# Kernel tuning notes

Measured on AMD Instinct MI355X. Metric: run time of the kernel, lower is better.

Reference implementation:

```python
import jax, jax.numpy as jnp
import numpy as np

B, H, Q, D = 8, 32, 1, 128
MAX_SEQ = 4096


def setup_inputs() -> dict:
    key = jax.random.key(0)
    k1, k2, k3, k4, k5 = jax.random.split(key, 5)
    return {
        "query": jax.random.normal(k1, (B, H, Q, D), dtype=jnp.float32),
        "key": jax.random.normal(k2, (B, H, Q, D), dtype=jnp.float32),
        "value": jax.random.normal(k3, (B, H, Q, D), dtype=jnp.float32),
        "cache_k": jax.random.normal(k4, (B, H, MAX_SEQ, D), dtype=jnp.float32),
        "cache_v": jax.random.normal(k5, (B, H, MAX_SEQ, D), dtype=jnp.float32),
        "cache_pos": MAX_SEQ - 1,  # decode step: cache nearly full
    }


def reference(query, key, value, cache_k, cache_v, cache_pos):
    # cache_pos is a static Python int (decode-step position, > 0).
    new_seq_len = key.shape[2]
    end_pos = cache_pos + new_seq_len
    # Slice-write new K/V into the cache (the torch module's in-place write).
    cache_k = cache_k.at[:, :, cache_pos:end_pos, :].set(key)
    cache_v = cache_v.at[:, :, cache_pos:end_pos, :].set(value)
    # Contiguous view of the valid prefix (the torch .contiguous() copy).
    full_k = cache_k[:, :, :end_pos, :]  # [B, H, end_pos, D]
    full_v = cache_v[:, :, :end_pos, :]
    # Decode path: SDPA with no mask, not causal.
    scale = 1.0 / jnp.sqrt(jnp.asarray(query.shape[-1], query.dtype))
    scores = jnp.einsum("bhqd,bhkd->bhqk", query, full_k) * scale
    attn = jax.nn.softmax(scores, axis=-1)
    out = jnp.einsum("bhqk,bhkd->bhqd", attn, full_v)
    return out
```

## Files before the change

### kernel.cpp

```cpp
#include <hip/hip_runtime.h>
#include <math.h>


#define BH_     256
#define D_      128
#define MAXS_   4096
#define NSPLIT_ 8
#define CHUNK_  (MAXS_ / NSPLIT_)
#define NWAVES_ 4
#define KPW_    (CHUNK_ / NWAVES_)
#define NPART_  (NWAVES_ * 2)
#define PSTRIDE_ (D_ + 2)

typedef float f4n __attribute__((ext_vector_type(4)));

static __device__ __forceinline__ f4n ntld4(const float* p) {
    return __builtin_nontemporal_load((const f4n*)p);
}

__global__ __launch_bounds__(256) void attn_partial_kernel(
    const float* __restrict__ q,
    const float* __restrict__ ck,
    const float* __restrict__ cv,
    const int*   __restrict__ cpos_p,
    float*       __restrict__ part)
{
    const int bh    = blockIdx.x;
    const int split = blockIdx.y;
    const int wave  = threadIdx.x >> 6;
    const int lane  = threadIdx.x & 63;
    const int half  = lane >> 5;
    const int li    = lane & 31;

    const int cpos = cpos_p[0];

    const float scale = 0.08838834764831845f;

    f4n qv = *(const f4n*)(q + (size_t)bh * D_ + li * 4);
    qv *= scale;

    const int base  = split * CHUNK_ + wave * KPW_;
    int limit = cpos - base;
    limit = limit < 0 ? 0 : (limit > KPW_ ? KPW_ : limit);

    float m = -INFINITY;
    float l = 0.0f;
    f4n   o = {0.0f, 0.0f, 0.0f, 0.0f};

    const float* __restrict__ kbase = ck + (size_t)bh * MAXS_ * D_;
    const float* __restrict__ vbase = cv + (size_t)bh * MAXS_ * D_;

#define UPDATE(KV, VV)                                                   \
    do {                                                                 \
        float dp = (KV).x * qv.x + (KV).y * qv.y                         \
                 + (KV).z * qv.z + (KV).w * qv.w;                        \
        dp += __shfl_xor(dp, 16);                                        \
        dp += __shfl_xor(dp, 8);                                         \
        dp += __shfl_xor(dp, 4);                                         \
        dp += __shfl_xor(dp, 2);                                         \
        dp += __shfl_xor(dp, 1);                                         \
        const float mn   = fmaxf(m, dp);                                 \
        const float corr = __expf(m - mn);                               \
        const float p    = __expf(dp - mn);                              \
        l   = l   * corr + p;                                            \
        o.x = o.x * corr + p * (VV).x;                                   \
        o.y = o.y * corr + p * (VV).y;                                   \
        o.z = o.z * corr + p * (VV).z;                                   \
        o.w = o.w * corr + p * (VV).w;                                   \
        m = mn;                                                          \
    } while (0)

    if (limit == KPW_) {
        const float* kp = kbase + (size_t)base * D_ + lane * 4;
        const float* vp = vbase + (size_t)base * D_ + lane * 4;
        f4n ka = ntld4(kp),        va = ntld4(vp);
        f4n kb = ntld4(kp + 256),  vb = ntld4(vp + 256);
        kp += 512; vp += 512;
        for (int i = 0; i < 31; ++i) {
            const f4n kc = ntld4(kp),       vc = ntld4(vp);
            const f4n kd = ntld4(kp + 256), vd = ntld4(vp + 256);
            kp += 512; vp += 512;
            UPDATE(ka, va);
            UPDATE(kb, vb);
            ka = kc; va = vc; kb = kd; vb = vd;
        }
        UPDATE(ka, va);
        UPDATE(kb, vb);
    } else {
        const int npairs = limit >> 1;
        for (int i = 0; i < npairs; ++i) {
            const int s0 = base + i * 2;
            const f4n kv = ntld4(kbase + (size_t)s0 * D_ + lane * 4);
            const f4n vv = ntld4(vbase + (size_t)s0 * D_ + lane * 4);
            UPDATE(kv, vv);
        }
        if ((limit & 1) && half == 0) {
            const int s = base + limit - 1;
            const f4n kv = ntld4(kbase + (size_t)s * D_ + li * 4);
            const f4n vv = ntld4(vbase + (size_t)s * D_ + li * 4);
            UPDATE(kv, vv);
        }
    }
#undef UPDATE

    __shared__ float s_o[NPART_][D_];
    __shared__ float s_m[NPART_];
    __shared__ float s_l[NPART_];
    const int pi = wave * 2 + half;
    *(f4n*)&s_o[pi][li * 4] = o;
    if (li == 0) { s_m[pi] = m; s_l[pi] = l; }
    __syncthreads();

    if (wave == 0) {
        float M = -INFINITY;
        #pragma unroll
        for (int p = 0; p < NPART_; ++p) M = fmaxf(M, s_m[p]);

        float* pp = part + ((size_t)bh * NSPLIT_ + split) * PSTRIDE_;
        const int d0 = lane * 2;
        if (M == -INFINITY) {
            pp[d0]     = 0.0f;
            pp[d0 + 1] = 0.0f;
            if (lane == 0) { pp[D_] = -INFINITY; pp[D_ + 1] = 0.0f; }
        } else {
            float L = 0.0f, a0 = 0.0f, a1 = 0.0f;
            #pragma unroll
            for (int p = 0; p < NPART_; ++p) {
                const float mp = s_m[p];
                const float w  = (mp == -INFINITY) ? 0.0f : __expf(mp - M);
                L  += w * s_l[p];
                a0 += w * s_o[p][d0];
                a1 += w * s_o[p][d0 + 1];
            }
            pp[d0]     = a0;
            pp[d0 + 1] = a1;
            if (lane == 0) { pp[D_] = M; pp[D_ + 1] = L; }
        }
    }
}

__global__ __launch_bounds__(64) void attn_combine_kernel(
    const float* __restrict__ q,
    const float* __restrict__ knew,
    const float* __restrict__ vnew,
    const float* __restrict__ part,
    float*       __restrict__ out)
{
    const int bh   = blockIdx.x;
    const int lane = threadIdx.x;
    const float scale = 0.08838834764831845f;

    const float2 qv = *(const float2*)(q    + (size_t)bh * D_ + lane * 2);
    const float2 kn = *(const float2*)(knew + (size_t)bh * D_ + lane * 2);
    float dp = qv.x * kn.x + qv.y * kn.y;
    #pragma unroll
    for (int off = 32; off > 0; off >>= 1) dp += __shfl_xor(dp, off);
    const float sc = dp * scale;

    const float* pb = part + (size_t)bh * NSPLIT_ * PSTRIDE_;

    float M = sc;
    #pragma unroll
    for (int p = 0; p < NSPLIT_; ++p) M = fmaxf(M, pb[p * PSTRIDE_ + D_]);

    const int d0 = lane * 2;
    const float2 vn = *(const float2*)(vnew + (size_t)bh * D_ + d0);
    const float wn = __expf(sc - M);
    float L  = wn;
    float a0 = wn * vn.x;
    float a1 = wn * vn.y;
    #pragma unroll
    for (int p = 0; p < NSPLIT_; ++p) {
        const float mp = pb[p * PSTRIDE_ + D_];
        const float w  = (mp == -INFINITY) ? 0.0f : __expf(mp - M);
        L  += w * pb[p * PSTRIDE_ + D_ + 1];
        a0 += w * pb[p * PSTRIDE_ + d0];
        a1 += w * pb[p * PSTRIDE_ + d0 + 1];
    }
    out[(size_t)bh * D_ + d0]     = a0 / L;
    out[(size_t)bh * D_ + d0 + 1] = a1 / L;
}

extern "C" void kernel_launch(void* const* d_in, const int* in_sizes, int n_in,
                              void* d_out, int out_size, void* d_ws, size_t ws_size,
                              hipStream_t stream) {
    const float* q    = (const float*)d_in[0];
    const float* knew = (const float*)d_in[1];
    const float* vnew = (const float*)d_in[2];
    const float* ck   = (const float*)d_in[3];
    const float* cv   = (const float*)d_in[4];
    const int*   cpos = (const int*)d_in[5];
    float* out  = (float*)d_out;
    float* part = (float*)d_ws;

    dim3 grid1(BH_, NSPLIT_);
    attn_partial_kernel<<<grid1, 256, 0, stream>>>(q, ck, cv, cpos, part);
    attn_combine_kernel<<<BH_, 64, 0, stream>>>(q, knew, vnew, part, out);
}
```

Measured before the change: 180.5 us.

## Fuse split-K partial and combine kernels into one 1024-thread block per head

```diff
diff --git a/kernel.cpp b/kernel.cpp
--- a/kernel.cpp
+++ b/kernel.cpp
@@ -2,15 +2,12 @@
 #include <math.h>
 
 
-#define BH_     256
-#define D_      128
-#define MAXS_   4096
-#define NSPLIT_ 8
-#define CHUNK_  (MAXS_ / NSPLIT_)
-#define NWAVES_ 4
-#define KPW_    (CHUNK_ / NWAVES_)
-#define NPART_  (NWAVES_ * 2)
-#define PSTRIDE_ (D_ + 2)
+#define BH_   256
+#define D_    128
+#define MAXS_ 4096
+#define NW_   16
+#define KPW_  (MAXS_ / NW_)
+#define NPART_ (NW_ * 2)
 
 typedef float f4n __attribute__((ext_vector_type(4)));
 
@@ -18,19 +15,20 @@
     return __builtin_nontemporal_load((const f4n*)p);
 }
 
-__global__ __launch_bounds__(256) void attn_partial_kernel(
+__global__ __launch_bounds__(1024) void attn_fused_kernel(
     const float* __restrict__ q,
+    const float* __restrict__ knew,
+    const float* __restrict__ vnew,
     const float* __restrict__ ck,
     const float* __restrict__ cv,
     const int*   __restrict__ cpos_p,
-    float*       __restrict__ part)
+    float*       __restrict__ out)
 {
-    const int bh    = blockIdx.x;
-    const int split = blockIdx.y;
-    const int wave  = threadIdx.x >> 6;
-    const int lane  = threadIdx.x & 63;
-    const int half  = lane >> 5;
-    const int li    = lane & 31;
+    const int bh   = blockIdx.x;
+    const int wave = threadIdx.x >> 6;
+    const int lane = threadIdx.x & 63;
+    const int half = lane >> 5;
+    const int li   = lane & 31;
 
     const int cpos = cpos_p[0];
 
@@ -39,7 +37,7 @@
     f4n qv = *(const f4n*)(q + (size_t)bh * D_ + li * 4);
     qv *= scale;
 
-    const int base  = split * CHUNK_ + wave * KPW_;
+    const int base  = wave * KPW_;
     int limit = cpos - base;
     limit = limit < 0 ? 0 : (limit > KPW_ ? KPW_ : limit);
 
@@ -76,7 +74,7 @@
         f4n ka = ntld4(kp),        va = ntld4(vp);
         f4n kb = ntld4(kp + 256),  vb = ntld4(vp + 256);
         kp += 512; vp += 512;
-        for (int i = 0; i < 31; ++i) {
+        for (int i = 0; i < (KPW_ / 4) - 1; ++i) {
             const f4n kc = ntld4(kp),       vc = ntld4(vp);
             const f4n kd = ntld4(kp + 256), vd = ntld4(vp + 256);
             kp += 512; vp += 512;
@@ -112,73 +110,33 @@
     __syncthreads();
 
     if (wave == 0) {
-        float M = -INFINITY;
+        const float2 q2 = *(const float2*)(q    + (size_t)bh * D_ + lane * 2);
+        const float2 k2 = *(const float2*)(knew + (size_t)bh * D_ + lane * 2);
+        float dp = q2.x * k2.x + q2.y * k2.y;
+        #pragma unroll
+        for (int off = 32; off > 0; off >>= 1) dp += __shfl_xor(dp, off);
+        const float sc = dp * scale;
+
+        float M = sc;
         #pragma unroll
         for (int p = 0; p < NPART_; ++p) M = fmaxf(M, s_m[p]);
 
-        float* pp = part + ((size_t)bh * NSPLIT_ + split) * PSTRIDE_;
         const int d0 = lane * 2;
-        if (M == -INFINITY) {
-            pp[d0]     = 0.0f;
-            pp[d0 + 1] = 0.0f;
-            if (lane == 0) { pp[D_] = -INFINITY; pp[D_ + 1] = 0.0f; }
-        } else {
-            float L = 0.0f, a0 = 0.0f, a1 = 0.0f;
-            #pragma unroll
-            for (int p = 0; p < NPART_; ++p) {
-                const float mp = s_m[p];
-                const float w  = (mp == -INFINITY) ? 0.0f : __expf(mp - M);
-                L  += w * s_l[p];
-                a0 += w * s_o[p][d0];
-                a1 += w * s_o[p][d0 + 1];
-            }
-            pp[d0]     = a0;
-            pp[d0 + 1] = a1;
-            if (lane == 0) { pp[D_] = M; pp[D_ + 1] = L; }
+        const float2 vn = *(const float2*)(vnew + (size_t)bh * D_ + d0);
+        const float wn = __expf(sc - M);
+        float L  = wn;
+        float a0 = wn * vn.x;
+        float a1 = wn * vn.y;
+        #pragma unroll
+        for (int p = 0; p < NPART_; ++p) {
+            const float w = __expf(s_m[p] - M);
+            L  += w * s_l[p];
+            a0 += w * s_o[p][d0];
+            a1 += w * s_o[p][d0 + 1];
         }
+        out[(size_t)bh * D_ + d0]     = a0 / L;
+        out[(size_t)bh * D_ + d0 + 1] = a1 / L;
     }
-}
-
-__global__ __launch_bounds__(64) void attn_combine_kernel(
-    const float* __restrict__ q,
-    const float* __restrict__ knew,
-    const float* __restrict__ vnew,
-    const float* __restrict__ part,
-    float*       __restrict__ out)
-{
-    const int bh   = blockIdx.x;
-    const int lane = threadIdx.x;
-    const float scale = 0.08838834764831845f;
-
-    const float2 qv = *(const float2*)(q    + (size_t)bh * D_ + lane * 2);
-    const float2 kn = *(const float2*)(knew + (size_t)bh * D_ + lane * 2);
-    float dp = qv.x * kn.x + qv.y * kn.y;
-    #pragma unroll
-    for (int off = 32; off > 0; off >>= 1) dp += __shfl_xor(dp, off);
-    const float sc = dp * scale;
-
-    const float* pb = part + (size_t)bh * NSPLIT_ * PSTRIDE_;
-
-    float M = sc;
-    #pragma unroll
-    for (int p = 0; p < NSPLIT_; ++p) M = fmaxf(M, pb[p * PSTRIDE_ + D_]);
-
-    const int d0 = lane * 2;
-    const float2 vn = *(const float2*)(vnew + (size_t)bh * D_ + d0);
-    const float wn = __expf(sc - M);
-    float L  = wn;
-    float a0 = wn * vn.x;
-    float a1 = wn * vn.y;
-    #pragma unroll
-    for (int p = 0; p < NSPLIT_; ++p) {
-        const float mp = pb[p * PSTRIDE_ + D_];
-        const float w  = (mp == -INFINITY) ? 0.0f : __expf(mp - M);
-        L  += w * pb[p * PSTRIDE_ + D_ + 1];
-        a0 += w * pb[p * PSTRIDE_ + d0];
-        a1 += w * pb[p * PSTRIDE_ + d0 + 1];
-    }
-    out[(size_t)bh * D_ + d0]     = a0 / L;
-    out[(size_t)bh * D_ + d0 + 1] = a1 / L;
 }
 
 extern "C" void kernel_launch(void* const* d_in, const int* in_sizes, int n_in,
@@ -190,10 +148,7 @@
     const float* ck   = (const float*)d_in[3];
     const float* cv   = (const float*)d_in[4];
     const int*   cpos = (const int*)d_in[5];
-    float* out  = (float*)d_out;
-    float* part = (float*)d_ws;
+    float* out = (float*)d_out;
 
-    dim3 grid1(BH_, NSPLIT_);
-    attn_partial_kernel<<<grid1, 256, 0, stream>>>(q, ck, cv, cpos, part);
-    attn_combine_kernel<<<BH_, 64, 0, stream>>>(q, knew, vnew, part, out);
+    attn_fused_kernel<<<BH_, NW_ * 64, 0, stream>>>(q, knew, vnew, ck, cv, cpos, out);
 }
```

Result: slower. 197.5 us (+9.4%).

## Fuse combine into partial kernel via last-block atomic counter

Applied to the files above, without the earlier changes.

```diff
diff --git a/kernel.cpp b/kernel.cpp
--- a/kernel.cpp
+++ b/kernel.cpp
@@ -11,6 +11,7 @@
 #define KPW_    (CHUNK_ / NWAVES_)
 #define NPART_  (NWAVES_ * 2)
 #define PSTRIDE_ (D_ + 2)
+#define PART_BYTES_ ((size_t)BH_ * NSPLIT_ * PSTRIDE_ * 4)
 
 typedef float f4n __attribute__((ext_vector_type(4)));
 
@@ -18,12 +19,16 @@
     return __builtin_nontemporal_load((const f4n*)p);
 }
 
-__global__ __launch_bounds__(256) void attn_partial_kernel(
+__global__ __launch_bounds__(256, 8) void attn_partial_fused_kernel(
     const float* __restrict__ q,
+    const float* __restrict__ knew,
+    const float* __restrict__ vnew,
     const float* __restrict__ ck,
     const float* __restrict__ cv,
     const int*   __restrict__ cpos_p,
-    float*       __restrict__ part)
+    float*       __restrict__ part,
+    unsigned int* __restrict__ ctr,
+    float*       __restrict__ out)
 {
     const int bh    = blockIdx.x;
     const int split = blockIdx.y;
@@ -76,7 +81,7 @@
         f4n ka = ntld4(kp),        va = ntld4(vp);
         f4n kb = ntld4(kp + 256),  vb = ntld4(vp + 256);
         kp += 512; vp += 512;
-        for (int i = 0; i < 31; ++i) {
+        for (int i = 0; i < (KPW_ / 4) - 1; ++i) {
             const f4n kc = ntld4(kp),       vc = ntld4(vp);
             const f4n kd = ntld4(kp + 256), vd = ntld4(vp + 256);
             kp += 512; vp += 512;
@@ -111,7 +116,9 @@
     if (li == 0) { s_m[pi] = m; s_l[pi] = l; }
     __syncthreads();
 
-    if (wave == 0) {
+    if (wave != 0) return;
+
+    {
         float M = -INFINITY;
         #pragma unroll
         for (int p = 0; p < NPART_; ++p) M = fmaxf(M, s_m[p]);
@@ -137,22 +144,18 @@
             if (lane == 0) { pp[D_] = M; pp[D_ + 1] = L; }
         }
     }
-}
-
-__global__ __launch_bounds__(64) void attn_combine_kernel(
-    const float* __restrict__ q,
-    const float* __restrict__ knew,
-    const float* __restrict__ vnew,
-    const float* __restrict__ part,
-    float*       __restrict__ out)
-{
-    const int bh   = blockIdx.x;
-    const int lane = threadIdx.x;
-    const float scale = 0.08838834764831845f;
-
-    const float2 qv = *(const float2*)(q    + (size_t)bh * D_ + lane * 2);
+
+    __threadfence();
+    int old = 0;
+    if (lane == 0) old = (int)atomicAdd(&ctr[bh], 1u);
+    old = __shfl(old, 0);
+    if (old != NSPLIT_ - 1) return;
+
+    __threadfence();
+
+    const float2 q2 = *(const float2*)(q    + (size_t)bh * D_ + lane * 2);
     const float2 kn = *(const float2*)(knew + (size_t)bh * D_ + lane * 2);
-    float dp = qv.x * kn.x + qv.y * kn.y;
+    float dp = q2.x * kn.x + q2.y * kn.y;
     #pragma unroll
     for (int off = 32; off > 0; off >>= 1) dp += __shfl_xor(dp, off);
     const float sc = dp * scale;
@@ -192,8 +195,11 @@
     const int*   cpos = (const int*)d_in[5];
     float* out  = (float*)d_out;
     float* part = (float*)d_ws;
-
-    dim3 grid1(BH_, NSPLIT_);
-    attn_partial_kernel<<<grid1, 256, 0, stream>>>(q, ck, cv, cpos, part);
-    attn_combine_kernel<<<BH_, 64, 0, stream>>>(q, knew, vnew, part, out);
+    unsigned int* ctr = (unsigned int*)((char*)d_ws + PART_BYTES_);
+
+    hipMemsetAsync(ctr, 0, BH_ * sizeof(unsigned int), stream);
+
+    dim3 grid(BH_, NSPLIT_);
+    attn_partial_fused_kernel<<<grid, 256, 0, stream>>>(
+        q, knew, vnew, ck, cv, cpos, part, ctr, out);
 }
```

Result: slower. 275.3 us (+52.6%).
